# Kernel tuning notes

Measured on AMD Instinct MI355X. Metric: run time of the kernel, lower is better.

Reference implementation:

```python
import jax, jax.numpy as jnp
import numpy as np

IN_FEATURES = 128
OUT_FEATURES = 128
N_HEADS = 64
BATCH = 8192


def setup_inputs() -> dict:
    key = jax.random.key(0)
    k_x, k_h, k_w = jax.random.split(key, 3)
    x = jax.random.normal(k_x, (BATCH, IN_FEATURES), dtype=jnp.float32)
    head_ix = jax.random.randint(k_h, (BATCH,), 0, N_HEADS, dtype=jnp.int64)
    stdv = 1.0 / np.sqrt(OUT_FEATURES)
    weight = jax.random.uniform(
        k_w, (N_HEADS, IN_FEATURES, OUT_FEATURES), dtype=jnp.float32,
        minval=-stdv, maxval=stdv)
    bias = jnp.zeros((N_HEADS, OUT_FEATURES), dtype=jnp.float32)
    return {"input": x, "weight": weight, "bias": bias, "head_ix": head_ix}


def reference(input, weight, bias, head_ix):
    # Gather per-row weight matrix [B, in, out] and bias [B, out], then
    # batched vector-matrix multiply: einsum('ab,abc->ac').
    w = weight[head_ix]            # [B, in, out]
    b = bias[head_ix]              # [B, out]
    out = jnp.einsum('bi,bio->bo', input, w) + b
    return out
```

## Files before the change

kernel.cpp:

```cpp
#include <hip/hip_runtime.h>

#define NHEADS 64
#define INF    128
#define OUTF   128
#define CAP    512
#define SPLITS 8
#define RROWS  4

__global__ __launch_bounds__(256) void bucket_kernel(
    const int* __restrict__ head_ix, int* __restrict__ counts,
    int* __restrict__ buckets, int n) {
  int r = blockIdx.x * 256 + threadIdx.x;
  if (r < n) {
    int h = head_ix[r];
    int pos = atomicAdd(&counts[h], 1);
    if (pos < CAP) buckets[h * CAP + pos] = r;
  }
}

__global__ __launch_bounds__(256) void head_gemv_kernel(
    const float* __restrict__ x, const float* __restrict__ W,
    const float* __restrict__ bias, const int* __restrict__ counts,
    const int* __restrict__ buckets, float* __restrict__ out) {
  __shared__ float Ws[INF * OUTF];

  const int h    = blockIdx.x;
  const int s    = blockIdx.y;
  const int tid  = threadIdx.x;
  const int wave = tid >> 6;
  const int lane = tid & 63;

  {
    const float4* Wg = (const float4*)(W + (size_t)h * (INF * OUTF));
    float4* Wl = (float4*)Ws;
#pragma unroll
    for (int t = 0; t < (INF * OUTF / 4) / 256; ++t)
      Wl[tid + t * 256] = Wg[tid + t * 256];
  }
  __syncthreads();

  const int cnt = min(counts[h], CAP);
  const float b0 = bias[h * OUTF + lane];
  const float b1 = bias[h * OUTF + 64 + lane];

  for (int base = (s * 4 + wave) * RROWS; base < cnt;
       base += SPLITS * 4 * RROWS) {
    int nr = cnt - base;
    if (nr > RROWS) nr = RROWS;

    int rows[RROWS];
#pragma unroll
    for (int r = 0; r < RROWS; ++r)
      rows[r] = (r < nr) ? buckets[h * CAP + base + r] : 0;

    float2 xv[RROWS];
#pragma unroll
    for (int r = 0; r < RROWS; ++r)
      xv[r] = ((const float2*)(x + (size_t)rows[r] * INF))[lane];

    float acc0[RROWS], acc1[RROWS];
#pragma unroll
    for (int r = 0; r < RROWS; ++r) { acc0[r] = b0; acc1[r] = b1; }

#pragma unroll 4
    for (int j = 0; j < INF / 2; ++j) {
      const int i0 = 2 * j, i1 = 2 * j + 1;
      float w0a = Ws[i0 * OUTF + lane];
      float w1a = Ws[i0 * OUTF + 64 + lane];
      float w0b = Ws[i1 * OUTF + lane];
      float w1b = Ws[i1 * OUTF + 64 + lane];
#pragma unroll
      for (int r = 0; r < RROWS; ++r) {
        float xix = __shfl(xv[r].x, j);
        float xiy = __shfl(xv[r].y, j);
        acc0[r] = fmaf(xix, w0a, acc0[r]);
        acc1[r] = fmaf(xix, w1a, acc1[r]);
        acc0[r] = fmaf(xiy, w0b, acc0[r]);
        acc1[r] = fmaf(xiy, w1b, acc1[r]);
      }
    }

#pragma unroll
    for (int r = 0; r < RROWS; ++r) {
      if (r < nr) {
        float* orow = out + (size_t)rows[r] * OUTF;
        orow[lane]      = acc0[r];
        orow[lane + 64] = acc1[r];
      }
    }
  }
}

extern "C" void kernel_launch(void* const* d_in, const int* in_sizes, int n_in,
                              void* d_out, int out_size, void* d_ws, size_t ws_size,
                              hipStream_t stream) {
  const float* x    = (const float*)d_in[0];
  const float* W    = (const float*)d_in[1];
  const float* bias = (const float*)d_in[2];
  const int*   hix  = (const int*)d_in[3];
  float* out = (float*)d_out;

  const int n = in_sizes[3];

  int* counts  = (int*)d_ws;
  int* buckets = counts + NHEADS;

  hipMemsetAsync(d_ws, 0, NHEADS * sizeof(int), stream);
  bucket_kernel<<<(n + 255) / 256, 256, 0, stream>>>(hix, counts, buckets, n);

  dim3 grid(NHEADS, SPLITS);
  head_gemv_kernel<<<grid, 256, 0, stream>>>(x, W, bias, counts, buckets, out);
}
```

Measured before the change: 99.65 us.

## Fuse head bucketing into GEMV kernel via wave ballot over head indices

Drops the memset and the atomic bucket kernel. Each wave now scans a fixed 256-row slice of head_ix with ballot and picks out, with ffs, the rows that match its block's head, up to four at a time. The x values are read as wave-uniform scalar loads instead of shuffles. This removes two extra launches and the global atomics, but it assumes n divides evenly into SPLITS*4*256-row slices. Any other batch size would silently skip rows.

Result: faster. 81.62 us (-18.1%).

```diff
diff --git a/kernel.cpp b/kernel.cpp
--- a/kernel.cpp
+++ b/kernel.cpp
@@ -3,90 +3,103 @@
 #define NHEADS 64
 #define INF    128
 #define OUTF   128
-#define CAP    512
 #define SPLITS 8
-#define RROWS  4
+#define BLOCK  256
 
-__global__ __launch_bounds__(256) void bucket_kernel(
-    const int* __restrict__ head_ix, int* __restrict__ counts,
-    int* __restrict__ buckets, int n) {
-  int r = blockIdx.x * 256 + threadIdx.x;
-  if (r < n) {
-    int h = head_ix[r];
-    int pos = atomicAdd(&counts[h], 1);
-    if (pos < CAP) buckets[h * CAP + pos] = r;
-  }
-}
-
-__global__ __launch_bounds__(256) void head_gemv_kernel(
+__global__ __launch_bounds__(BLOCK) void fused_headgemv(
     const float* __restrict__ x, const float* __restrict__ W,
-    const float* __restrict__ bias, const int* __restrict__ counts,
-    const int* __restrict__ buckets, float* __restrict__ out) {
+    const float* __restrict__ bias, const int* __restrict__ hix,
+    float* __restrict__ out, int n) {
   __shared__ float Ws[INF * OUTF];
 
   const int h    = blockIdx.x;
   const int s    = blockIdx.y;
   const int tid  = threadIdx.x;
-  const int wave = tid >> 6;
   const int lane = tid & 63;
+  const int w    = tid >> 6;
 
   {
     const float4* Wg = (const float4*)(W + (size_t)h * (INF * OUTF));
     float4* Wl = (float4*)Ws;
 #pragma unroll
-    for (int t = 0; t < (INF * OUTF / 4) / 256; ++t)
-      Wl[tid + t * 256] = Wg[tid + t * 256];
+    for (int t = 0; t < (INF * OUTF / 4) / BLOCK; ++t)
+      Wl[tid + t * BLOCK] = Wg[tid + t * BLOCK];
   }
   __syncthreads();
 
-  const int cnt = min(counts[h], CAP);
   const float b0 = bias[h * OUTF + lane];
   const float b1 = bias[h * OUTF + 64 + lane];
 
-  for (int base = (s * 4 + wave) * RROWS; base < cnt;
-       base += SPLITS * 4 * RROWS) {
-    int nr = cnt - base;
-    if (nr > RROWS) nr = RROWS;
+  const int range = n / SPLITS;
+  const int sub   = s * range + w * (range / 4);
+  unsigned long long mask[4];
+#pragma unroll
+  for (int c = 0; c < 4; ++c) {
+    int r  = sub + c * 64 + lane;
+    int hv = (r < n) ? hix[r] : -1;
+    mask[c] = __ballot(hv == h);
+  }
 
-    int rows[RROWS];
+  int c = 0;
+  unsigned long long m = mask[0];
+  for (;;) {
+    int rows[4];
+    int nr = 0;
+    while (nr < 4) {
+      while (m == 0ull && c < 3) m = mask[++c];
+      if (m == 0ull) break;
+      int b = __ffsll((unsigned long long)m) - 1;
+      m &= (m - 1);
+      rows[nr++] = __builtin_amdgcn_readfirstlane(sub + c * 64 + b);
+    }
+    if (nr == 0) break;
 #pragma unroll
-    for (int r = 0; r < RROWS; ++r)
-      rows[r] = (r < nr) ? buckets[h * CAP + base + r] : 0;
+    for (int r = nr; r < 4; ++r) rows[r] = rows[0];
 
-    float2 xv[RROWS];
+    const float* xr0 = x + (size_t)rows[0] * INF;
+    const float* xr1 = x + (size_t)rows[1] * INF;
+    const float* xr2 = x + (size_t)rows[2] * INF;
+    const float* xr3 = x + (size_t)rows[3] * INF;
+
+    float acc00 = b0, acc01 = b0, acc02 = b0, acc03 = b0;
+    float acc10 = b1, acc11 = b1, acc12 = b1, acc13 = b1;
+
+    for (int kc = 0; kc < INF / 8; ++kc) {
+      float xs0[8], xs1[8], xs2[8], xs3[8];
 #pragma unroll
-    for (int r = 0; r < RROWS; ++r)
-      xv[r] = ((const float2*)(x + (size_t)rows[r] * INF))[lane];
-
-    float acc0[RROWS], acc1[RROWS];
+      for (int i = 0; i < 8; ++i) {
+        xs0[i] = xr0[kc * 8 + i];
+        xs1[i] = xr1[kc * 8 + i];
+        xs2[i] = xr2[kc * 8 + i];
+        xs3[i] = xr3[kc * 8 + i];
+      }
 #pragma unroll
-    for (int r = 0; r < RROWS; ++r) { acc0[r] = b0; acc1[r] = b1; }
-
-#pragma unroll 4
-    for (int j = 0; j < INF / 2; ++j) {
-      const int i0 = 2 * j, i1 = 2 * j + 1;
-      float w0a = Ws[i0 * OUTF + lane];
-      float w1a = Ws[i0 * OUTF + 64 + lane];
-      float w0b = Ws[i1 * OUTF + lane];
-      float w1b = Ws[i1 * OUTF + 64 + lane];
-#pragma unroll
-      for (int r = 0; r < RROWS; ++r) {
-        float xix = __shfl(xv[r].x, j);
-        float xiy = __shfl(xv[r].y, j);
-        acc0[r] = fmaf(xix, w0a, acc0[r]);
-        acc1[r] = fmaf(xix, w1a, acc1[r]);
-        acc0[r] = fmaf(xiy, w0b, acc0[r]);
-        acc1[r] = fmaf(xiy, w1b, acc1[r]);
+      for (int i = 0; i < 8; ++i) {
+        const int k = kc * 8 + i;
+        float w0 = Ws[k * OUTF + lane];
+        float w1 = Ws[k * OUTF + 64 + lane];
+        acc00 = fmaf(xs0[i], w0, acc00); acc10 = fmaf(xs0[i], w1, acc10);
+        acc01 = fmaf(xs1[i], w0, acc01); acc11 = fmaf(xs1[i], w1, acc11);
+        acc02 = fmaf(xs2[i], w0, acc02); acc12 = fmaf(xs2[i], w1, acc12);
+        acc03 = fmaf(xs3[i], w0, acc03); acc13 = fmaf(xs3[i], w1, acc13);
       }
     }
 
-#pragma unroll
-    for (int r = 0; r < RROWS; ++r) {
-      if (r < nr) {
-        float* orow = out + (size_t)rows[r] * OUTF;
-        orow[lane]      = acc0[r];
-        orow[lane + 64] = acc1[r];
-      }
+    {
+      float* o = out + (size_t)rows[0] * OUTF;
+      o[lane] = acc00; o[64 + lane] = acc10;
+    }
+    if (nr > 1) {
+      float* o = out + (size_t)rows[1] * OUTF;
+      o[lane] = acc01; o[64 + lane] = acc11;
+    }
+    if (nr > 2) {
+      float* o = out + (size_t)rows[2] * OUTF;
+      o[lane] = acc02; o[64 + lane] = acc12;
+    }
+    if (nr > 3) {
+      float* o = out + (size_t)rows[3] * OUTF;
+      o[lane] = acc03; o[64 + lane] = acc13;
     }
   }
 }
@@ -102,12 +115,6 @@
 
   const int n = in_sizes[3];
 
-  int* counts  = (int*)d_ws;
-  int* buckets = counts + NHEADS;
-
-  hipMemsetAsync(d_ws, 0, NHEADS * sizeof(int), stream);
-  bucket_kernel<<<(n + 255) / 256, 256, 0, stream>>>(hix, counts, buckets, n);
-
   dim3 grid(NHEADS, SPLITS);
-  head_gemv_kernel<<<grid, 256, 0, stream>>>(x, W, bias, counts, buckets, out);
+  fused_headgemv<<<grid, BLOCK, 0, stream>>>(x, W, bias, hix, out, n);
 }
```
